# Optimization experiments

Measured on AMD Instinct MI355X. Metric: run time of the kernel, lower is better.

## Reference

```python
import jax, jax.numpy as jnp
import numpy as np

SPACING = (1.0, 1.0, 1.0)  # uniform grid spacing per axis


def setup_inputs() -> dict:
    key = jax.random.key(0)
    values = jax.random.normal(key, (4, 256, 256, 256), dtype=jnp.float32)
    return {"values": values}


def reference(values):
    # Central difference with periodic boundaries on each of the last 3 axes.
    # For periodic BCs, grad[i] = (v[i+1] - v[i-1]) / (2h) for ALL i (wrap-around),
    # which is exactly jnp.roll(-1) - jnp.roll(+1); this matches the original's
    # interior slices plus its explicit periodic boundary writes.
    hx, hy, hz = SPACING
    gx = (jnp.roll(values, -1, axis=-3) - jnp.roll(values, 1, axis=-3)) / (2.0 * hx)
    gy = (jnp.roll(values, -1, axis=-2) - jnp.roll(values, 1, axis=-2)) / (2.0 * hy)
    gz = (jnp.roll(values, -1, axis=-1) - jnp.roll(values, 1, axis=-1)) / (2.0 * hz)
    # Stack component axis just before the 3 spatial dims: [..., 3, nx, ny, nz]
    return jnp.stack([gx, gy, gz], axis=-4)
```

## Files before the change

kernel.cpp:

```cpp
#include <hip/hip_runtime.h>


__global__ __launch_bounds__(256) void fdgrad_kernel(
    const float* __restrict__ vin, float* __restrict__ vout) {
    const unsigned tid = blockIdx.x * 256u + threadIdx.x;

    const unsigned z4 = tid & 63u;
    const unsigned y  = (tid >> 6) & 255u;
    const unsigned x  = (tid >> 14) & 255u;
    const unsigned b  = tid >> 22;

    const float4* __restrict__ vin4 = reinterpret_cast<const float4*>(vin);
    float4* __restrict__ vout4      = reinterpret_cast<float4*>(vout);

    const unsigned xp = (x == 255u) ? 0u : x + 1u;
    const unsigned xm = (x == 0u) ? 255u : x - 1u;
    const unsigned yp = (y == 255u) ? 0u : y + 1u;
    const unsigned ym = (y == 0u) ? 255u : y - 1u;

    const unsigned base_b = b << 22;
    const unsigned idx_c  = base_b + (x << 14) + (y << 6) + z4;
    const unsigned idx_xp = base_b + (xp << 14) + (y << 6) + z4;
    const unsigned idx_xm = base_b + (xm << 14) + (y << 6) + z4;
    const unsigned idx_yp = base_b + (x << 14) + (yp << 6) + z4;
    const unsigned idx_ym = base_b + (x << 14) + (ym << 6) + z4;

    const float4 c  = vin4[idx_c];
    const float4 vxp = vin4[idx_xp];
    const float4 vxm = vin4[idx_xm];
    const float4 vyp = vin4[idx_yp];
    const float4 vym = vin4[idx_ym];

    const unsigned z0 = z4 << 2;
    const unsigned row = (b << 24) + (x << 16) + (y << 8);
    const float zm = vin[row + ((z4 == 0u) ? 255u : z0 - 1u)];
    const float zp = vin[row + ((z4 == 63u) ? 0u : z0 + 4u)];

    float4 gx, gy, gz;
    gx.x = (vxp.x - vxm.x) * 0.5f;
    gx.y = (vxp.y - vxm.y) * 0.5f;
    gx.z = (vxp.z - vxm.z) * 0.5f;
    gx.w = (vxp.w - vxm.w) * 0.5f;

    gy.x = (vyp.x - vym.x) * 0.5f;
    gy.y = (vyp.y - vym.y) * 0.5f;
    gy.z = (vyp.z - vym.z) * 0.5f;
    gy.w = (vyp.w - vym.w) * 0.5f;

    gz.x = (c.y - zm) * 0.5f;
    gz.y = (c.z - c.x) * 0.5f;
    gz.z = (c.w - c.y) * 0.5f;
    gz.w = (zp - c.z) * 0.5f;

    const unsigned spatial = (x << 14) + (y << 6) + z4;
    vout4[((b * 3u + 0u) << 22) + spatial] = gx;
    vout4[((b * 3u + 1u) << 22) + spatial] = gy;
    vout4[((b * 3u + 2u) << 22) + spatial] = gz;
}

extern "C" void kernel_launch(void* const* d_in, const int* in_sizes, int n_in,
                              void* d_out, int out_size, void* d_ws, size_t ws_size,
                              hipStream_t stream) {
    const float* vin = (const float*)d_in[0];
    float* vout = (float*)d_out;
    fdgrad_kernel<<<65536, 256, 0, stream>>>(vin, vout);
}
```

Measured before the change: 961.4 us.

## Stream along x with register sliding window, wave shuffles for z halo, nontemporal stores

Each thread now walks 16 consecutive x planes and keeps the previous, current and next x values in registers, so each x neighbour is loaded once instead of three times. The z neighbours come from wave shuffles instead of extra scalar global loads, which works because a 64-lane wave covers exactly one 256-float z row. Output is written with nontemporal stores to keep it from polluting the cache, and the grid shrinks 16x. The risk is lower parallelism per launch and a serial dependence chain per thread, while the y-neighbour loads still rely on cache hits.

```diff
diff --git a/kernel.cpp b/kernel.cpp
--- a/kernel.cpp
+++ b/kernel.cpp
@@ -1,61 +1,68 @@
 #include <hip/hip_runtime.h>
 
+
+typedef float f32x4 __attribute__((ext_vector_type(4)));
 
 __global__ __launch_bounds__(256) void fdgrad_kernel(
     const float* __restrict__ vin, float* __restrict__ vout) {
     const unsigned tid = blockIdx.x * 256u + threadIdx.x;
 
-    const unsigned z4 = tid & 63u;
-    const unsigned y  = (tid >> 6) & 255u;
-    const unsigned x  = (tid >> 14) & 255u;
-    const unsigned b  = tid >> 22;
+    const unsigned z4  = tid & 63u;
+    const unsigned y   = (tid >> 6) & 255u;
+    const unsigned seg = (tid >> 14) & 15u;
+    const unsigned b   = tid >> 18;
 
-    const float4* __restrict__ vin4 = reinterpret_cast<const float4*>(vin);
-    float4* __restrict__ vout4      = reinterpret_cast<float4*>(vout);
+    const f32x4* __restrict__ vin4 = reinterpret_cast<const f32x4*>(vin);
+    f32x4* __restrict__ vout4      = reinterpret_cast<f32x4*>(vout);
 
-    const unsigned xp = (x == 255u) ? 0u : x + 1u;
-    const unsigned xm = (x == 0u) ? 255u : x - 1u;
-    const unsigned yp = (y == 255u) ? 0u : y + 1u;
-    const unsigned ym = (y == 0u) ? 255u : y - 1u;
+    const unsigned yp = (y + 1u) & 255u;
+    const unsigned ym = (y + 255u) & 255u;
 
     const unsigned base_b = b << 22;
-    const unsigned idx_c  = base_b + (x << 14) + (y << 6) + z4;
-    const unsigned idx_xp = base_b + (xp << 14) + (y << 6) + z4;
-    const unsigned idx_xm = base_b + (xm << 14) + (y << 6) + z4;
-    const unsigned idx_yp = base_b + (x << 14) + (yp << 6) + z4;
-    const unsigned idx_ym = base_b + (x << 14) + (ym << 6) + z4;
+    const unsigned ofs_c  = (y  << 6) + z4;
+    const unsigned ofs_yp = (yp << 6) + z4;
+    const unsigned ofs_ym = (ym << 6) + z4;
 
-    const float4 c  = vin4[idx_c];
-    const float4 vxp = vin4[idx_xp];
-    const float4 vxm = vin4[idx_xm];
-    const float4 vyp = vin4[idx_yp];
-    const float4 vym = vin4[idx_ym];
+    const unsigned out_gx = (b * 3u + 0u) << 22;
+    const unsigned out_gy = (b * 3u + 1u) << 22;
+    const unsigned out_gz = (b * 3u + 2u) << 22;
 
-    const unsigned z0 = z4 << 2;
-    const unsigned row = (b << 24) + (x << 16) + (y << 8);
-    const float zm = vin[row + ((z4 == 0u) ? 255u : z0 - 1u)];
-    const float zp = vin[row + ((z4 == 63u) ? 0u : z0 + 4u)];
+    const unsigned lane = threadIdx.x & 63u;
+    const int lm = (int)((lane + 63u) & 63u);
+    const int lp = (int)((lane + 1u)  & 63u);
 
-    float4 gx, gy, gz;
-    gx.x = (vxp.x - vxm.x) * 0.5f;
-    gx.y = (vxp.y - vxm.y) * 0.5f;
-    gx.z = (vxp.z - vxm.z) * 0.5f;
-    gx.w = (vxp.w - vxm.w) * 0.5f;
+    unsigned x = seg << 4;
 
-    gy.x = (vyp.x - vym.x) * 0.5f;
-    gy.y = (vyp.y - vym.y) * 0.5f;
-    gy.z = (vyp.z - vym.z) * 0.5f;
-    gy.w = (vyp.w - vym.w) * 0.5f;
+    f32x4 vm = vin4[base_b + (((x + 255u) & 255u) << 14) + ofs_c];
+    f32x4 vc = vin4[base_b + (x << 14) + ofs_c];
 
-    gz.x = (c.y - zm) * 0.5f;
-    gz.y = (c.z - c.x) * 0.5f;
-    gz.z = (c.w - c.y) * 0.5f;
-    gz.w = (zp - c.z) * 0.5f;
+#pragma unroll 4
+    for (int i = 0; i < 16; ++i) {
+        const unsigned xn = (x + 1u) & 255u;
+        const f32x4 vp  = vin4[base_b + (xn << 14) + ofs_c];
+        const f32x4 vyp = vin4[base_b + (x  << 14) + ofs_yp];
+        const f32x4 vym = vin4[base_b + (x  << 14) + ofs_ym];
 
-    const unsigned spatial = (x << 14) + (y << 6) + z4;
-    vout4[((b * 3u + 0u) << 22) + spatial] = gx;
-    vout4[((b * 3u + 1u) << 22) + spatial] = gy;
-    vout4[((b * 3u + 2u) << 22) + spatial] = gz;
+        const float zm = __shfl(vc.w, lm, 64);
+        const float zp = __shfl(vc.x, lp, 64);
+
+        f32x4 gx, gy, gz;
+        gx = (vp  - vm)  * 0.5f;
+        gy = (vyp - vym) * 0.5f;
+        gz.x = (vc.y - zm)   * 0.5f;
+        gz.y = (vc.z - vc.x) * 0.5f;
+        gz.z = (vc.w - vc.y) * 0.5f;
+        gz.w = (zp   - vc.z) * 0.5f;
+
+        const unsigned spatial = (x << 14) + ofs_c;
+        __builtin_nontemporal_store(gx, &vout4[out_gx + spatial]);
+        __builtin_nontemporal_store(gy, &vout4[out_gy + spatial]);
+        __builtin_nontemporal_store(gz, &vout4[out_gz + spatial]);
+
+        vm = vc;
+        vc = vp;
+        x  = xn;
+    }
 }
 
 extern "C" void kernel_launch(void* const* d_in, const int* in_sizes, int n_in,
@@ -63,5 +70,5 @@
                               hipStream_t stream) {
     const float* vin = (const float*)d_in[0];
     float* vout = (float*)d_out;
-    fdgrad_kernel<<<65536, 256, 0, stream>>>(vin, vout);
+    fdgrad_kernel<<<4096, 256, 0, stream>>>(vin, vout);
 }
```

Result: no change. 957.1 us (-0.4%).
